# Kernel optimization log

Hardware: AMD Instinct MI355X
Metric: run time of the kernel (lower is better)

The kernel has to match this reference:

```python
import jax, jax.numpy as jnp
import numpy as np

D_MODEL = 1024
NHEAD = 16
D_HEAD = D_MODEL // NHEAD
B, L = 2, 2048


def setup_inputs() -> dict:
    key = jax.random.key(0)
    ks = jax.random.split(key, 11)
    s = 1.0 / np.sqrt(D_MODEL)
    return {
        "Q": jax.random.normal(ks[0], (B, L, D_MODEL), jnp.float32),
        "K": jax.random.normal(ks[1], (B, L, D_MODEL), jnp.float32),
        "V": jax.random.normal(ks[2], (B, L, D_MODEL), jnp.float32),
        "Wq": jax.random.normal(ks[3], (D_MODEL, D_MODEL), jnp.float32) * s,
        "bq": jax.random.normal(ks[4], (D_MODEL,), jnp.float32) * 0.01,
        "Wk": jax.random.normal(ks[5], (D_MODEL, D_MODEL), jnp.float32) * s,
        "bk": jax.random.normal(ks[6], (D_MODEL,), jnp.float32) * 0.01,
        "Wv": jax.random.normal(ks[7], (D_MODEL, D_MODEL), jnp.float32) * s,
        "bv": jax.random.normal(ks[8], (D_MODEL,), jnp.float32) * 0.01,
        "Wo": jax.random.normal(ks[9], (D_MODEL, D_MODEL), jnp.float32) * s,
        "bo": jax.random.normal(ks[10], (D_MODEL,), jnp.float32) * 0.01,
    }


def reference(Q, K, V, Wq, bq, Wk, bk, Wv, bv, Wo, bo):
    b, l, _ = Q.shape
    # QKV linear projections (nn.Linear: x @ W.T + b), then split into heads
    q = (Q @ Wq.T + bq).reshape(b, l, NHEAD, D_HEAD)
    k = (K @ Wk.T + bk).reshape(b, l, NHEAD, D_HEAD)
    v = (V @ Wv.T + bv).reshape(b, l, NHEAD, D_HEAD)
    # scaled dot-product attention: softmax(QK^T / sqrt(d_head)) V
    scale = jnp.asarray(1.0 / np.sqrt(D_HEAD), q.dtype)
    scores = jnp.einsum("bqhd,bkhd->bhqk", q, k) * scale  # [B,H,L,L]
    attn = jax.nn.softmax(scores, axis=-1)
    out = jnp.einsum("bhqk,bkhd->bqhd", attn, v)  # [B,L,H,Dh]
    out = out.reshape(b, l, D_MODEL)  # concat heads
    return out @ Wo.T + bo
```

## Files before the change

kernel.cpp:

```cpp
#include <hip/hip_runtime.h>
#include <cstdint>
#include <cstddef>

#define DM 1024
#define NH 16
#define DH 64
#define NB 2
#define SQ 2048
#define MT (NB*SQ)

typedef float  f32x4 __attribute__((ext_vector_type(4)));
typedef short  s16x8 __attribute__((ext_vector_type(8)));
typedef short  s16x4 __attribute__((ext_vector_type(4)));

__device__ __forceinline__ unsigned short f2bf(float x) {
    unsigned int u = __float_as_uint(x);
    unsigned int lsb = (u >> 16) & 1u;
    u += 0x7fffu + lsb;
    return (unsigned short)(u >> 16);
}

__device__ __forceinline__ void gload16(const void* g, void* l) {
    __builtin_amdgcn_global_load_lds(
        (const __attribute__((address_space(1))) void*)g,
        (__attribute__((address_space(3))) void*)l,
        16, 0, 0);
}

__global__ __launch_bounds__(256) void castk(const float* __restrict__ in,
                                             unsigned short* __restrict__ out, int n) {
    int i = (blockIdx.x * 256 + threadIdx.x) * 4;
    if (i >= n) return;
    float4 a = *reinterpret_cast<const float4*>(in + i);
    s16x4 r;
    r[0] = (short)f2bf(a.x);
    r[1] = (short)f2bf(a.y);
    r[2] = (short)f2bf(a.z);
    r[3] = (short)f2bf(a.w);
    *reinterpret_cast<s16x4*>(out + i) = r;
}

__device__ __forceinline__ void gemm_core(const unsigned short* __restrict__ A,
                                          const unsigned short* __restrict__ Bm,
                                          int m0, int n0, int t,
                                          unsigned short (*As)[64],
                                          unsigned short (*Bs)[64],
                                          f32x4 acc[4][4]) {
    const int lane = t & 63, w = t >> 6;
    const int wm = (w >> 1) * 64, wn = (w & 1) * 64;
    const int lo = lane & 15, hi = lane >> 4;

    for (int k0 = 0; k0 < DM; k0 += 64) {
#pragma unroll
        for (int i = 0; i < 4; i++) {
            int c = i * 256 + t;
            int r = c >> 3, col = (c & 7) * 8;
            gload16(A  + (size_t)(m0 + r) * DM + k0 + col, &As[r][col]);
            gload16(Bm + (size_t)(n0 + r) * DM + k0 + col, &Bs[r][col]);
        }
        asm volatile("s_waitcnt vmcnt(0)" ::: "memory");
        __syncthreads();

#pragma unroll
        for (int kk = 0; kk < 64; kk += 32) {
            s16x8 a[4], b[4];
#pragma unroll
            for (int mi = 0; mi < 4; mi++)
                a[mi] = *reinterpret_cast<const s16x8*>(&As[wm + mi * 16 + lo][kk + hi * 8]);
#pragma unroll
            for (int ni = 0; ni < 4; ni++)
                b[ni] = *reinterpret_cast<const s16x8*>(&Bs[wn + ni * 16 + lo][kk + hi * 8]);
#pragma unroll
            for (int mi = 0; mi < 4; mi++)
#pragma unroll
                for (int ni = 0; ni < 4; ni++)
                    acc[mi][ni] = __builtin_amdgcn_mfma_f32_16x16x32_bf16(
                        a[mi], b[ni], acc[mi][ni], 0, 0, 0);
        }
        __syncthreads();
    }
}

__global__ __launch_bounds__(256, 3) void gemm_qkv(
    const unsigned short* __restrict__ Qb, const unsigned short* __restrict__ Kb,
    const unsigned short* __restrict__ Vb,
    const unsigned short* __restrict__ Wq, const unsigned short* __restrict__ Wk,
    const unsigned short* __restrict__ Wv,
    const float* __restrict__ bq, const float* __restrict__ bk, const float* __restrict__ bv,
    unsigned short* __restrict__ qp, unsigned short* __restrict__ kp,
    unsigned short* __restrict__ vt) {
    __shared__ __align__(16) unsigned short As[128][64];
    __shared__ __align__(16) unsigned short Bs[128][64];
    const int t = threadIdx.x;
    const int z = blockIdx.z;
    const unsigned short* A    = (z == 0) ? Qb : (z == 1) ? Kb : Vb;
    const unsigned short* Bm   = (z == 0) ? Wq : (z == 1) ? Wk : Wv;
    const float*          bias = (z == 0) ? bq : (z == 1) ? bk : bv;
    const int m0 = blockIdx.y * 128, n0 = blockIdx.x * 128;

    f32x4 acc[4][4] = {};
    gemm_core(A, Bm, m0, n0, t, As, Bs, acc);

    const int lane = t & 63, w = t >> 6;
    const int wm = (w >> 1) * 64, wn = (w & 1) * 64;
    const int lo = lane & 15, hi = lane >> 4;

    if (z < 2) {
        unsigned short* C = z ? kp : qp;
        const float scale = z ? 1.0f : 0.125f;
#pragma unroll
        for (int mi = 0; mi < 4; mi++)
#pragma unroll
            for (int ni = 0; ni < 4; ni++) {
                int cc = n0 + wn + ni * 16 + lo;
                float bb = bias[cc];
#pragma unroll
                for (int j = 0; j < 4; j++) {
                    int rr = m0 + wm + mi * 16 + hi * 4 + j;
                    C[(size_t)rr * DM + cc] = f2bf((acc[mi][ni][j] + bb) * scale);
                }
            }
    } else {
#pragma unroll
        for (int mi = 0; mi < 4; mi++)
#pragma unroll
            for (int ni = 0; ni < 4; ni++) {
                int cc = n0 + wn + ni * 16 + lo;
                float bb = bias[cc];
#pragma unroll
                for (int j = 0; j < 4; j++) {
                    int rr = m0 + wm + mi * 16 + hi * 4 + j;
                    size_t idx = ((size_t)(rr >> 11) * DM + cc) * SQ + (rr & (SQ - 1));
                    vt[idx] = f2bf(acc[mi][ni][j] + bb);
                }
            }
    }
}

__global__ __launch_bounds__(256, 3) void gemm_out(
    const unsigned short* __restrict__ Ao, const unsigned short* __restrict__ Wo,
    const float* __restrict__ bo, float* __restrict__ Cout) {
    __shared__ __align__(16) unsigned short As[128][64];
    __shared__ __align__(16) unsigned short Bs[128][64];
    const int t = threadIdx.x;
    const int m0 = blockIdx.y * 128, n0 = blockIdx.x * 128;

    f32x4 acc[4][4] = {};
    gemm_core(Ao, Wo, m0, n0, t, As, Bs, acc);

    const int lane = t & 63, w = t >> 6;
    const int wm = (w >> 1) * 64, wn = (w & 1) * 64;
    const int lo = lane & 15, hi = lane >> 4;
#pragma unroll
    for (int mi = 0; mi < 4; mi++)
#pragma unroll
        for (int ni = 0; ni < 4; ni++) {
            int cc = n0 + wn + ni * 16 + lo;
            float bb = bo[cc];
#pragma unroll
            for (int j = 0; j < 4; j++) {
                int rr = m0 + wm + mi * 16 + hi * 4 + j;
                Cout[(size_t)rr * DM + cc] = acc[mi][ni][j] + bb;
            }
        }
}

__global__ __launch_bounds__(256, 2) void attn_k(
    const unsigned short* __restrict__ qp, const unsigned short* __restrict__ kp,
    const unsigned short* __restrict__ vt, unsigned short* __restrict__ ao) {
    __shared__ __align__(16) unsigned short Qs[128][64];
    __shared__ __align__(16) unsigned short Ks[128][64];
    __shared__ __align__(16) unsigned short Vs[64][128];
    __shared__ __align__(16) unsigned short Ps[4][32][128];

    const int t = threadIdx.x;
    const int lane = t & 63, w = t >> 6;
    const int lo = lane & 15, hi = lane >> 4;
    const int q0 = blockIdx.x * 128;
    const int bh = blockIdx.y;
    const int b = bh >> 4, h = bh & 15;

#pragma unroll
    for (int i = 0; i < 4; i++) {
        int c = i * 256 + t;
        int r = c >> 3, col = ((c & 7) ^ (r & 7)) * 8;
        gload16(qp + (size_t)(b * SQ + q0 + r) * DM + h * DH + col, &Qs[r][(c & 7) * 8]);
    }

    float mrow[2][4], lrow[2][4];
#pragma unroll
    for (int mi = 0; mi < 2; mi++)
#pragma unroll
        for (int j = 0; j < 4; j++) { mrow[mi][j] = -1e30f; lrow[mi][j] = 0.0f; }
    f32x4 oacc[2][4] = {};

    for (int kt = 0; kt < SQ; kt += 128) {
#pragma unroll
        for (int i = 0; i < 4; i++) {
            int c = i * 256 + t;
            int r = c >> 3, col = ((c & 7) ^ (r & 7)) * 8;
            gload16(kp + (size_t)(b * SQ + kt + r) * DM + h * DH + col, &Ks[r][(c & 7) * 8]);
        }
#pragma unroll
        for (int i = 0; i < 4; i++) {
            int c = i * 256 + t;
            int r = c >> 4, col = ((c & 15) ^ (r & 15)) * 8;
            gload16(vt + (size_t)(bh * DH + r) * SQ + kt + col, &Vs[r][(c & 15) * 8]);
        }
        asm volatile("s_waitcnt vmcnt(0)" ::: "memory");
        __syncthreads();

        f32x4 sacc[2][8] = {};
#pragma unroll
        for (int kk = 0; kk < 64; kk += 32) {
            s16x8 aq[2];
#pragma unroll
            for (int mi = 0; mi < 2; mi++) {
                int qr = w * 32 + mi * 16 + lo;
                aq[mi] = *reinterpret_cast<const s16x8*>(
                    &Qs[qr][((kk / 8 + hi) ^ (qr & 7)) * 8]);
            }
#pragma unroll
            for (int cf = 0; cf < 8; cf++) {
                int kr = cf * 16 + lo;
                s16x8 bk = *reinterpret_cast<const s16x8*>(
                    &Ks[kr][((kk / 8 + hi) ^ (kr & 7)) * 8]);
#pragma unroll
                for (int mi = 0; mi < 2; mi++)
                    sacc[mi][cf] = __builtin_amdgcn_mfma_f32_16x16x32_bf16(
                        aq[mi], bk, sacc[mi][cf], 0, 0, 0);
            }
        }

#pragma unroll
        for (int mi = 0; mi < 2; mi++) {
#pragma unroll
            for (int j = 0; j < 4; j++) {
                float mx = sacc[mi][0][j];
#pragma unroll
                for (int cf = 1; cf < 8; cf++) mx = fmaxf(mx, sacc[mi][cf][j]);
#pragma unroll
                for (int d = 1; d < 16; d <<= 1) mx = fmaxf(mx, __shfl_xor(mx, d));
                float mold = mrow[mi][j];
                float mnew = fmaxf(mold, mx);
                float fs = __expf(mold - mnew);
                mrow[mi][j] = mnew;
                float psum = 0.0f;
                int prow = mi * 16 + hi * 4 + j;
                int pm = prow & 15;
#pragma unroll
                for (int cf = 0; cf < 8; cf++) {
                    float p = __expf(sacc[mi][cf][j] - mnew);
                    psum += p;
                    Ps[w][prow][(((cf * 2 + (lo >> 3)) ^ pm) * 8) + (lo & 7)] = f2bf(p);
                }
#pragma unroll
                for (int d = 1; d < 16; d <<= 1) psum += __shfl_xor(psum, d);
                lrow[mi][j] = lrow[mi][j] * fs + psum;
#pragma unroll
                for (int ni = 0; ni < 4; ni++) oacc[mi][ni][j] *= fs;
            }
        }

#pragma unroll
        for (int kc = 0; kc < 4; kc++) {
            s16x8 pa[2];
#pragma unroll
            for (int mi = 0; mi < 2; mi++) {
                int pr = mi * 16 + lo;
                pa[mi] = *reinterpret_cast<const s16x8*>(
                    &Ps[w][pr][((kc * 4 + hi) ^ (pr & 15)) * 8]);
            }
#pragma unroll
            for (int ni = 0; ni < 4; ni++) {
                int vr = ni * 16 + lo;
                s16x8 bvf = *reinterpret_cast<const s16x8*>(
                    &Vs[vr][((kc * 4 + hi) ^ (vr & 15)) * 8]);
#pragma unroll
                for (int mi = 0; mi < 2; mi++)
                    oacc[mi][ni] = __builtin_amdgcn_mfma_f32_16x16x32_bf16(
                        pa[mi], bvf, oacc[mi][ni], 0, 0, 0);
            }
        }
        __syncthreads();
    }

#pragma unroll
    for (int mi = 0; mi < 2; mi++)
#pragma unroll
        for (int j = 0; j < 4; j++) {
            float inv = 1.0f / lrow[mi][j];
            int rr = q0 + w * 32 + mi * 16 + hi * 4 + j;
#pragma unroll
            for (int ni = 0; ni < 4; ni++) {
                int cc = ni * 16 + lo;
                ao[(size_t)(b * SQ + rr) * DM + h * DH + cc] = f2bf(oacc[mi][ni][j] * inv);
            }
        }
}

extern "C" void kernel_launch(void* const* d_in, const int* in_sizes, int n_in,
                              void* d_out, int out_size, void* d_ws, size_t ws_size,
                              hipStream_t stream) {
    const float* Q  = (const float*)d_in[0];
    const float* K  = (const float*)d_in[1];
    const float* V  = (const float*)d_in[2];
    const float* Wq = (const float*)d_in[3];
    const float* bq = (const float*)d_in[4];
    const float* Wk = (const float*)d_in[5];
    const float* bk = (const float*)d_in[6];
    const float* Wv = (const float*)d_in[7];
    const float* bv = (const float*)d_in[8];
    const float* Wo = (const float*)d_in[9];
    const float* bo = (const float*)d_in[10];

    char* ws = (char*)d_ws;
    size_t off = 0;
    auto alloc = [&](size_t bytes) {
        void* p = ws + off;
        off += (bytes + 255) & ~(size_t)255;
        return p;
    };
    const size_t XB = (size_t)MT * DM * 2;
    const size_t WB = (size_t)DM * DM * 2;
    unsigned short* qb  = (unsigned short*)alloc(XB);
    unsigned short* kb  = (unsigned short*)alloc(XB);
    unsigned short* vb  = (unsigned short*)alloc(XB);
    unsigned short* wqb = (unsigned short*)alloc(WB);
    unsigned short* wkb = (unsigned short*)alloc(WB);
    unsigned short* wvb = (unsigned short*)alloc(WB);
    unsigned short* wob = (unsigned short*)alloc(WB);
    unsigned short* qp  = (unsigned short*)alloc(XB);
    unsigned short* kp  = (unsigned short*)alloc(XB);
    unsigned short* vtp = (unsigned short*)alloc(XB);
    unsigned short* ao  = (unsigned short*)alloc(XB);

    castk<<<dim3(MT * DM / 1024), 256, 0, stream>>>(Q, qb, MT * DM);
    castk<<<dim3(MT * DM / 1024), 256, 0, stream>>>(K, kb, MT * DM);
    castk<<<dim3(MT * DM / 1024), 256, 0, stream>>>(V, vb, MT * DM);
    castk<<<dim3(DM * DM / 1024), 256, 0, stream>>>(Wq, wqb, DM * DM);
    castk<<<dim3(DM * DM / 1024), 256, 0, stream>>>(Wk, wkb, DM * DM);
    castk<<<dim3(DM * DM / 1024), 256, 0, stream>>>(Wv, wvb, DM * DM);
    castk<<<dim3(DM * DM / 1024), 256, 0, stream>>>(Wo, wob, DM * DM);

    gemm_qkv<<<dim3(DM / 128, MT / 128, 3), 256, 0, stream>>>(
        qb, kb, vb, wqb, wkb, wvb, bq, bk, bv, qp, kp, vtp);

    attn_k<<<dim3(SQ / 128, NB * NH), 256, 0, stream>>>(qp, kp, vtp, ao);

    gemm_out<<<dim3(DM / 128, MT / 128), 256, 0, stream>>>(ao, wob, bo, (float*)d_out);
}
```

Before: 279.8 us.

## Compute transposed attention scores with 32x32 MFMA and keep P in registers

The attention kernel now computes S^T = K·Q^T with 32x32x16 bf16 MFMA, so each lane owns one query row. The row max and sum then need only a single cross-half shuffle instead of 16-lane butterfly reductions. The P tile is packed to bf16 and exchanged between lane halves by shuffles, then fed straight into the PV MFMA, which removes the Ps shared-memory round trip. Q fragments are cached in registers once, and log2(e) is folded into the Q scale so exp2f can be used. The cost is more register pressure from the f32x16 accumulators and the shuffle permutation logic.

```diff
diff --git a/kernel.cpp b/kernel.cpp
--- a/kernel.cpp
+++ b/kernel.cpp
@@ -9,7 +9,8 @@
 #define SQ 2048
 #define MT (NB*SQ)
 
-typedef float  f32x4 __attribute__((ext_vector_type(4)));
+typedef float  f32x4  __attribute__((ext_vector_type(4)));
+typedef float  f32x16 __attribute__((ext_vector_type(16)));
 typedef short  s16x8 __attribute__((ext_vector_type(8)));
 typedef short  s16x4 __attribute__((ext_vector_type(4)));
 
@@ -107,7 +108,7 @@
 
     if (z < 2) {
         unsigned short* C = z ? kp : qp;
-        const float scale = z ? 1.0f : 0.125f;
+        const float scale = z ? 1.0f : 0.18033688011112042f;
 #pragma unroll
         for (int mi = 0; mi < 4; mi++)
 #pragma unroll
@@ -171,11 +172,10 @@
     __shared__ __align__(16) unsigned short Qs[128][64];
     __shared__ __align__(16) unsigned short Ks[128][64];
     __shared__ __align__(16) unsigned short Vs[64][128];
-    __shared__ __align__(16) unsigned short Ps[4][32][128];
 
     const int t = threadIdx.x;
     const int lane = t & 63, w = t >> 6;
-    const int lo = lane & 15, hi = lane >> 4;
+    const int l5 = lane & 31, hb = lane >> 5;
     const int q0 = blockIdx.x * 128;
     const int bh = blockIdx.y;
     const int b = bh >> 4, h = bh & 15;
@@ -187,12 +187,9 @@
         gload16(qp + (size_t)(b * SQ + q0 + r) * DM + h * DH + col, &Qs[r][(c & 7) * 8]);
     }
 
-    float mrow[2][4], lrow[2][4];
-#pragma unroll
-    for (int mi = 0; mi < 2; mi++)
-#pragma unroll
-        for (int j = 0; j < 4; j++) { mrow[mi][j] = -1e30f; lrow[mi][j] = 0.0f; }
-    f32x4 oacc[2][4] = {};
+    float mrow = -1e30f, lrow = 0.0f;
+    f32x16 oaccT[2] = {};
+    s16x8 qfrag[4];
 
     for (int kt = 0; kt < SQ; kt += 128) {
 #pragma unroll
@@ -210,92 +207,101 @@
         asm volatile("s_waitcnt vmcnt(0)" ::: "memory");
         __syncthreads();
 
-        f32x4 sacc[2][8] = {};
-#pragma unroll
-        for (int kk = 0; kk < 64; kk += 32) {
-            s16x8 aq[2];
-#pragma unroll
-            for (int mi = 0; mi < 2; mi++) {
-                int qr = w * 32 + mi * 16 + lo;
-                aq[mi] = *reinterpret_cast<const s16x8*>(
-                    &Qs[qr][((kk / 8 + hi) ^ (qr & 7)) * 8]);
-            }
-#pragma unroll
-            for (int cf = 0; cf < 8; cf++) {
-                int kr = cf * 16 + lo;
-                s16x8 bk = *reinterpret_cast<const s16x8*>(
-                    &Ks[kr][((kk / 8 + hi) ^ (kr & 7)) * 8]);
-#pragma unroll
-                for (int mi = 0; mi < 2; mi++)
-                    sacc[mi][cf] = __builtin_amdgcn_mfma_f32_16x16x32_bf16(
-                        aq[mi], bk, sacc[mi][cf], 0, 0, 0);
-            }
-        }
-
-#pragma unroll
-        for (int mi = 0; mi < 2; mi++) {
-#pragma unroll
-            for (int j = 0; j < 4; j++) {
-                float mx = sacc[mi][0][j];
-#pragma unroll
-                for (int cf = 1; cf < 8; cf++) mx = fmaxf(mx, sacc[mi][cf][j]);
-#pragma unroll
-                for (int d = 1; d < 16; d <<= 1) mx = fmaxf(mx, __shfl_xor(mx, d));
-                float mold = mrow[mi][j];
-                float mnew = fmaxf(mold, mx);
-                float fs = __expf(mold - mnew);
-                mrow[mi][j] = mnew;
-                float psum = 0.0f;
-                int prow = mi * 16 + hi * 4 + j;
-                int pm = prow & 15;
-#pragma unroll
-                for (int cf = 0; cf < 8; cf++) {
-                    float p = __expf(sacc[mi][cf][j] - mnew);
-                    psum += p;
-                    Ps[w][prow][(((cf * 2 + (lo >> 3)) ^ pm) * 8) + (lo & 7)] = f2bf(p);
+        if (kt == 0) {
+#pragma unroll
+            for (int kk = 0; kk < 4; kk++) {
+                int qr = w * 32 + l5;
+                qfrag[kk] = *reinterpret_cast<const s16x8*>(
+                    &Qs[qr][((kk * 2 + hb) ^ (qr & 7)) * 8]);
+            }
+        }
+
+        f32x16 sT[4] = {};
+#pragma unroll
+        for (int ks = 0; ks < 4; ks++) {
+#pragma unroll
+            for (int kk = 0; kk < 4; kk++) {
+                int kr = ks * 32 + l5;
+                s16x8 kf = *reinterpret_cast<const s16x8*>(
+                    &Ks[kr][((kk * 2 + hb) ^ (kr & 7)) * 8]);
+                sT[ks] = __builtin_amdgcn_mfma_f32_32x32x16_bf16(
+                    kf, qfrag[kk], sT[ks], 0, 0, 0);
+            }
+        }
+
+        float mx = -3.0e38f;
+#pragma unroll
+        for (int ks = 0; ks < 4; ks++) {
+            float a0 = fmaxf(fmaxf(sT[ks][0], sT[ks][1]), fmaxf(sT[ks][2], sT[ks][3]));
+            float a1 = fmaxf(fmaxf(sT[ks][4], sT[ks][5]), fmaxf(sT[ks][6], sT[ks][7]));
+            float a2 = fmaxf(fmaxf(sT[ks][8], sT[ks][9]), fmaxf(sT[ks][10], sT[ks][11]));
+            float a3 = fmaxf(fmaxf(sT[ks][12], sT[ks][13]), fmaxf(sT[ks][14], sT[ks][15]));
+            mx = fmaxf(mx, fmaxf(fmaxf(a0, a1), fmaxf(a2, a3)));
+        }
+        mx = fmaxf(mx, __shfl_xor(mx, 32));
+        float mnew = fmaxf(mrow, mx);
+        float fs = exp2f(mrow - mnew);
+        mrow = mnew;
+        float ps = 0.0f;
+#pragma unroll
+        for (int ks = 0; ks < 4; ks++)
+#pragma unroll
+            for (int r = 0; r < 16; r++) {
+                float e = exp2f(sT[ks][r] - mnew);
+                sT[ks][r] = e;
+                ps += e;
+            }
+        ps += __shfl_xor(ps, 32);
+        lrow = lrow * fs + ps;
+        oaccT[0] *= fs;
+        oaccT[1] *= fs;
+
+#pragma unroll
+        for (int ks = 0; ks < 4; ks++) {
+            unsigned int pw0[4], pw1[4];
+#pragma unroll
+            for (int m = 0; m < 4; m++) {
+                pw0[m] = (unsigned int)f2bf(sT[ks][4 * m]) |
+                         ((unsigned int)f2bf(sT[ks][4 * m + 1]) << 16);
+                pw1[m] = (unsigned int)f2bf(sT[ks][4 * m + 2]) |
+                         ((unsigned int)f2bf(sT[ks][4 * m + 3]) << 16);
+            }
+#pragma unroll
+            for (int tt = 0; tt < 2; tt++) {
+                unsigned int s0 = hb ? pw0[2 * tt] : pw0[2 * tt + 1];
+                unsigned int s1 = hb ? pw1[2 * tt] : pw1[2 * tt + 1];
+                unsigned int r0 = __shfl_xor(s0, 32);
+                unsigned int r1 = __shfl_xor(s1, 32);
+                union { unsigned int u[4]; s16x8 v; } uu;
+                if (hb == 0) { uu.u[0] = pw0[2 * tt]; uu.u[1] = pw1[2 * tt];
+                               uu.u[2] = r0;          uu.u[3] = r1; }
+                else         { uu.u[0] = r0;          uu.u[1] = r1;
+                               uu.u[2] = pw0[2 * tt + 1]; uu.u[3] = pw1[2 * tt + 1]; }
+                s16x8 pf = uu.v;
+#pragma unroll
+                for (int dblk = 0; dblk < 2; dblk++) {
+                    int vr = dblk * 32 + l5;
+                    int sl = ((ks * 2 + tt) * 2 + hb) ^ (vr & 15);
+                    s16x8 vf = *reinterpret_cast<const s16x8*>(&Vs[vr][sl * 8]);
+                    oaccT[dblk] = __builtin_amdgcn_mfma_f32_32x32x16_bf16(
+                        vf, pf, oaccT[dblk], 0, 0, 0);
                 }
-#pragma unroll
-                for (int d = 1; d < 16; d <<= 1) psum += __shfl_xor(psum, d);
-                lrow[mi][j] = lrow[mi][j] * fs + psum;
-#pragma unroll
-                for (int ni = 0; ni < 4; ni++) oacc[mi][ni][j] *= fs;
-            }
-        }
-
-#pragma unroll
-        for (int kc = 0; kc < 4; kc++) {
-            s16x8 pa[2];
-#pragma unroll
-            for (int mi = 0; mi < 2; mi++) {
-                int pr = mi * 16 + lo;
-                pa[mi] = *reinterpret_cast<const s16x8*>(
-                    &Ps[w][pr][((kc * 4 + hi) ^ (pr & 15)) * 8]);
-            }
-#pragma unroll
-            for (int ni = 0; ni < 4; ni++) {
-                int vr = ni * 16 + lo;
-                s16x8 bvf = *reinterpret_cast<const s16x8*>(
-                    &Vs[vr][((kc * 4 + hi) ^ (vr & 15)) * 8]);
-#pragma unroll
-                for (int mi = 0; mi < 2; mi++)
-                    oacc[mi][ni] = __builtin_amdgcn_mfma_f32_16x16x32_bf16(
-                        pa[mi], bvf, oacc[mi][ni], 0, 0, 0);
             }
         }
         __syncthreads();
     }
 
-#pragma unroll
-    for (int mi = 0; mi < 2; mi++)
-#pragma unroll
-        for (int j = 0; j < 4; j++) {
-            float inv = 1.0f / lrow[mi][j];
-            int rr = q0 + w * 32 + mi * 16 + hi * 4 + j;
-#pragma unroll
-            for (int ni = 0; ni < 4; ni++) {
-                int cc = ni * 16 + lo;
-                ao[(size_t)(b * SQ + rr) * DM + h * DH + cc] = f2bf(oacc[mi][ni][j] * inv);
-            }
+    float inv = 1.0f / lrow;
+    size_t rowbase = (size_t)(b * SQ + q0 + w * 32 + l5) * DM + h * DH;
+#pragma unroll
+    for (int dblk = 0; dblk < 2; dblk++)
+#pragma unroll
+        for (int g = 0; g < 4; g++) {
+            s16x4 st;
+#pragma unroll
+            for (int j = 0; j < 4; j++)
+                st[j] = (short)f2bf(oaccT[dblk][4 * g + j] * inv);
+            *reinterpret_cast<s16x4*>(&ao[rowbase + dblk * 32 + 8 * g + 4 * hb]) = st;
         }
 }
 
```

New measurement: 269.2 us. 1.04x faster.
